# Kernel optimization log

Measured on AMD Instinct MI355X. Metric: run time of the kernel, lower is better.

The kernel has to match this reference:

```python
import jax, jax.numpy as jnp
import numpy as np

K = 20
EPS = 1e-5
SLOPE = 0.2


def setup_inputs() -> dict:
    key = jax.random.key(0)
    k1, k2 = jax.random.split(key, 2)
    B, C, N, O = 2, 64, 8192, 64
    x = jax.random.normal(k1, (B, C, N), dtype=jnp.float32)
    W = jax.random.normal(k2, (O, 2 * C), dtype=jnp.float32) * 0.05  # Conv2d 1x1, bias=False
    gamma = jnp.ones((O,), dtype=jnp.float32)
    beta = jnp.zeros((O,), dtype=jnp.float32)
    return {"x": x, "W": W, "gamma": gamma, "beta": beta}


def reference(x, W, gamma, beta):
    # x: (B, C, N)
    B, C, N = x.shape
    xt = jnp.swapaxes(x, 1, 2)  # (B, N, C)

    # --- get_GraphFeatures: KNN by negative squared euclidean distance ---
    inner = jnp.einsum('bnc,bmc->bnm', xt, xt)          # (B, N, N)
    sq = jnp.sum(xt * xt, axis=-1)                      # (B, N)
    neg_dist = 2.0 * inner - sq[:, :, None] - sq[:, None, :]
    _, idx = jax.lax.top_k(neg_dist, K)                 # (B, N, K) int32

    # gather neighbor features: (B, N, K, C)
    nbr = jax.vmap(lambda pts, i: pts[i])(xt, idx)
    center = xt[:, :, None, :]                          # (B, N, 1, C)
    # edge feature: concat(x_j - x_i, x_i) -> (B, N, K, 2C)
    edge = jnp.concatenate([nbr - center, jnp.broadcast_to(center, nbr.shape)], axis=-1)

    # --- 1x1 conv (pointwise GEMM) -> (B, O, N, K) ---
    h = jnp.einsum('bnkf,of->bonk', edge, W)

    # --- BatchNorm2d (training-mode batch stats over B, N, K per channel) ---
    mean = jnp.mean(h, axis=(0, 2, 3), keepdims=True)
    var = jnp.var(h, axis=(0, 2, 3), keepdims=True)
    h = (h - mean) * jax.lax.rsqrt(var + EPS)
    h = h * gamma[None, :, None, None] + beta[None, :, None, None]

    # --- LeakyReLU(0.2) + max over neighbors ---
    h = jnp.where(h >= 0, h, SLOPE * h)
    return jnp.max(h, axis=-1)                          # (B, O, N)
```

## Files before the change

### kernel.cpp

```cpp
#include <hip/hip_runtime.h>
#include <cfloat>

#define BB 2
#define NN 8192
#define OO 64
#define KK 20
#define QB 128
#define MS 16
#define CHUNK 512
#define CAPQ 192
#define RB 8
#define RBS 9

using f16x8  = __attribute__((ext_vector_type(8))) _Float16;
using f32x16 = __attribute__((ext_vector_type(16))) float;
typedef unsigned long long u64;

#define XH_OFF ((size_t)0)
#define XL_OFF (XH_OFF + (size_t)BB*NN*32)
#define SQ_OFF (XL_OFF + (size_t)BB*NN*32)
#define Y1_OFF (SQ_OFF + (size_t)BB*NN)
#define Y2_OFF (Y1_OFF + (size_t)BB*NN*64)
#define TH_OFF (Y2_OFF + (size_t)BB*NN*64)
#define CN_OFF (TH_OFF + (size_t)BB*NN)
#define TL_OFF (CN_OFF + (size_t)BB*NN)
#define CA_OFF (TL_OFF + (size_t)2*BB*NN*KK)
#define IX_OFF (CA_OFF + (size_t)BB*NN*CAPQ*2)
#define HX_OFF (IX_OFF + (size_t)BB*NN*KK)
#define HN_OFF (HX_OFF + (size_t)BB*NN*64)
#define ST_OFF (HN_OFF + (size_t)BB*NN*64)

__device__ __forceinline__ size_t frag_off(int b, int tile, int t, int lane) {
    return ((((size_t)b * (NN / 32) + tile) * 4 + t) * 64 + lane) * 8;
}

__device__ __forceinline__ unsigned fmap(float f) {
    unsigned u = __float_as_uint(f);
    return (u & 0x80000000u) ? ~u : (u | 0x80000000u);
}

__device__ __forceinline__ void sort16(float* v) {
#pragma unroll
    for (int k = 2; k <= 16; k <<= 1) {
#pragma unroll
        for (int j = k >> 1; j > 0; j >>= 1) {
#pragma unroll
            for (int i = 0; i < 16; ++i) {
                int l = i ^ j;
                if (l > i) {
                    bool up = ((i & k) == 0);
                    float mn = fminf(v[i], v[l]);
                    float mx = fmaxf(v[i], v[l]);
                    v[i] = up ? mn : mx;
                    v[l] = up ? mx : mn;
                }
            }
        }
    }
}
__device__ __forceinline__ void bmerge32(float* A) {
#pragma unroll
    for (int j = 16; j > 0; j >>= 1) {
#pragma unroll
        for (int i = 0; i < 32; ++i) {
            if ((i & j) == 0) {
                float mn = fminf(A[i], A[i | j]);
                float mx = fmaxf(A[i], A[i | j]);
                A[i] = mn;
                A[i | j] = mx;
            }
        }
    }
}
__device__ __forceinline__ void merge32_16(float* A, const float* B) {
#pragma unroll
    for (int i = 16; i < 32; ++i) A[i] = fminf(A[i], B[31 - i]);
    bmerge32(A);
}
__device__ __forceinline__ void merge32_32(float* A, const float* B) {
    float t[32];
#pragma unroll
    for (int i = 0; i < 32; ++i) t[i] = fminf(A[i], B[31 - i]);
    bmerge32(t);
#pragma unroll
    for (int i = 0; i < 32; ++i) A[i] = t[i];
}

__device__ __forceinline__ void load_atile(const _Float16* __restrict__ xh,
                                           const _Float16* __restrict__ xl,
                                           int b, int ptile, int lane,
                                           f16x8* Ah, f16x8* Al) {
#pragma unroll
    for (int t = 0; t < 4; ++t) {
        size_t o = frag_off(b, ptile, t, lane);
        Ah[t] = *(const f16x8*)&xh[o];
        Al[t] = *(const f16x8*)&xl[o];
    }
}

__device__ __forceinline__ void dist_from_frags(const f16x8* Ah, const f16x8* Al,
                                                const float* sqs, int sbase, int kh,
                                                const f16x8* Qh, const f16x8* Ql,
                                                float* dv) {
    f32x16 c0, c1;
#pragma unroll
    for (int r2 = 0; r2 < 4; ++r2) {
        float4 sv = *(const float4*)&sqs[sbase + 8 * r2 + 4 * kh];
        c0[4 * r2 + 0] = sv.x;
        c0[4 * r2 + 1] = sv.y;
        c0[4 * r2 + 2] = sv.z;
        c0[4 * r2 + 3] = sv.w;
    }
#pragma unroll
    for (int i = 0; i < 16; ++i) c1[i] = 0.f;
#pragma unroll
    for (int t = 0; t < 4; ++t) {
        c0 = __builtin_amdgcn_mfma_f32_32x32x16_f16(Ah[t], Qh[t], c0, 0, 0, 0);
        c1 = __builtin_amdgcn_mfma_f32_32x32x16_f16(Ah[t], Ql[t], c1, 0, 0, 0);
        c1 = __builtin_amdgcn_mfma_f32_32x32x16_f16(Al[t], Qh[t], c1, 0, 0, 0);
    }
#pragma unroll
    for (int i = 0; i < 16; ++i)
        dv[i] = fmaf(-2.f, c0[i], -9.765625e-4f * c1[i]);
}

__device__ __forceinline__ void load_qfrag(const _Float16* __restrict__ xh,
                                           const _Float16* __restrict__ xl,
                                           int b, int qbase, int lane,
                                           f16x8* Qh, f16x8* Ql) {
    const int qtile = qbase >> 5;
#pragma unroll
    for (int t = 0; t < 4; ++t) {
        size_t o = frag_off(b, qtile, t, lane);
        Qh[t] = *(const f16x8*)&xh[o];
        Ql[t] = *(const f16x8*)&xl[o];
    }
}

__global__ void __launch_bounds__(256, 2)
kA(const float* __restrict__ x, const float* __restrict__ W,
   float* __restrict__ ws) {
    __shared__ __align__(16) float w1s[32 * 64];
    __shared__ __align__(16) float w2s[32 * 64];
    __shared__ float xs[64 * 65];
    __shared__ float tb[64 * 33];
    const int bb = blockIdx.z;
    const int og = blockIdx.y;
    const int obase = og * 32;
    const int nbase = blockIdx.x * 64;
    const int tn = threadIdx.x & 63, tq = threadIdx.x >> 6;

    for (int i = threadIdx.x; i < 2048; i += 256) {
        int ol = i >> 6, c = i & 63;
        float a = W[(obase + ol) * 128 + c];
        float d = W[(obase + ol) * 128 + 64 + c];
        w1s[i] = a;
        w2s[i] = d - a;
    }
    for (int i = threadIdx.x; i < 4096; i += 256) {
        int c = i >> 6, nl = i & 63;
        xs[c * 65 + nl] = x[((size_t)bb * 64 + c) * NN + nbase + nl];
    }
    if (og == 0) {
        if (blockIdx.x == 0 && bb == 0 && threadIdx.x < 128)
            ws[ST_OFF + threadIdx.x] = 0.f;
        int gid = (bb * 128 + blockIdx.x) * 256 + threadIdx.x;
        if (gid < BB * NN) ((int*)(ws + CN_OFF))[gid] = 0;
    }
    __syncthreads();

    float xc[64];
#pragma unroll
    for (int c = 0; c < 64; ++c) xc[c] = xs[c * 65 + tn];

    if (og == 0 && tq == 0) {
        float sqv = 0.f;
#pragma unroll
        for (int c = 0; c < 64; ++c) sqv = fmaf(xc[c], xc[c], sqv);
        int n = nbase + tn;
        ws[SQ_OFF + (size_t)bb * NN + n] = sqv;
        _Float16* xh = (_Float16*)(ws + XH_OFF);
        _Float16* xl = (_Float16*)(ws + XL_OFF);
        int tile = n >> 5, r = n & 31;
#pragma unroll
        for (int t = 0; t < 4; ++t) {
#pragma unroll
            for (int kh = 0; kh < 2; ++kh) {
                f16x8 vh, vl;
#pragma unroll
                for (int j = 0; j < 8; ++j) {
                    float v = xc[t * 16 + kh * 8 + j];
                    _Float16 h = (_Float16)v;
                    vh[j] = h;
                    vl[j] = (_Float16)((v - (float)h) * 2048.f);
                }
                size_t o = frag_off(bb, tile, t, kh * 32 + r);
                *(f16x8*)&xh[o] = vh;
                *(f16x8*)&xl[o] = vl;
            }
        }
    }

    float a1v[8], a2v[8];
#pragma unroll
    for (int o2 = 0; o2 < 8; ++o2) {
        int ol = tq * 8 + o2;
        const float4* w1v = (const float4*)&w1s[ol * 64];
        const float4* w2v = (const float4*)&w2s[ol * 64];
        float a1 = 0.f, a2 = 0.f;
#pragma unroll
        for (int c4 = 0; c4 < 16; ++c4) {
            float4 v1 = w1v[c4];
            float4 v2 = w2v[c4];
            a1 = fmaf(v1.x, xc[4*c4],   a1);
            a1 = fmaf(v1.y, xc[4*c4+1], a1);
            a1 = fmaf(v1.z, xc[4*c4+2], a1);
            a1 = fmaf(v1.w, xc[4*c4+3], a1);
            a2 = fmaf(v2.x, xc[4*c4],   a2);
            a2 = fmaf(v2.y, xc[4*c4+1], a2);
            a2 = fmaf(v2.z, xc[4*c4+2], a2);
            a2 = fmaf(v2.w, xc[4*c4+3], a2);
        }
        a1v[o2] = a1;
        a2v[o2] = a2;
    }

    const int lo = threadIdx.x & 31;
    const int lp = (threadIdx.x >> 5) & 1;
#pragma unroll
    for (int o2 = 0; o2 < 8; ++o2)
        tb[tn * 33 + tq * 8 + o2] = a1v[o2];
    __syncthreads();
#pragma unroll
    for (int j = 0; j < 8; ++j) {
        int r = tq * 16 + 2 * j + lp;
        ws[Y1_OFF + ((size_t)bb * NN + nbase + r) * 64 + obase + lo] = tb[r * 33 + lo];
    }
    __syncthreads();
#pragma unroll
    for (int o2 = 0; o2 < 8; ++o2)
        tb[tn * 33 + tq * 8 + o2] = a2v[o2];
    __syncthreads();
#pragma unroll
    for (int j = 0; j < 8; ++j) {
        int r = tq * 16 + 2 * j + lp;
        ws[Y2_OFF + ((size_t)bb * NN + nbase + r) * 64 + obase + lo] = tb[r * 33 + lo];
    }
}

__global__ void __launch_bounds__(256, 3)
kT(const _Float16* __restrict__ xh, const _Float16* __restrict__ xl,
   const float* __restrict__ sq, float* __restrict__ thrL) {
    __shared__ float mrg[32 * 128];
    __shared__ __align__(16) float sqs[1024];
    const int tid  = threadIdx.x;
    const int lane = tid & 63;
    const int wv   = tid >> 6;
    const int qcol = lane & 31;
    const int kh   = lane >> 5;
    const int b     = blockIdx.y >> 1;
    const int s     = blockIdx.y & 1;
    const int qbase = blockIdx.x * 32;

    for (int i = tid; i < 1024; i += 256)
        sqs[i] = -0.5f * sq[(size_t)b * NN + s * 1024 + i];

    f16x8 Qh[4], Ql[4];
    load_qfrag(xh, xl, b, qbase, lane, Qh, Ql);
    __syncthreads();

    float dk[32];
#pragma unroll
    for (int i = 0; i < 32; ++i) dk[i] = FLT_MAX;

    const int p0 = s * 1024 + wv * 256;
    for (int pt = p0; pt < p0 + 256; pt += 32) {
        f16x8 Ah[4], Al[4];
        load_atile(xh, xl, b, pt >> 5, lane, Ah, Al);
        float dv[16];
        dist_from_frags(Ah, Al, sqs, pt - s * 1024, kh, Qh, Ql, dv);
        float m16 = dv[0];
#pragma unroll
        for (int i = 1; i < 16; ++i) m16 = fminf(m16, dv[i]);
        if (__any(m16 < dk[KK - 1])) {
            sort16(dv);
            merge32_16(dk, dv);
        }
    }

    {
        float B[32];
#pragma unroll
        for (int j = 0; j < 32; ++j) B[j] = __shfl(dk[j], lane | 32);
        merge32_32(dk, B);
    }
    if (kh == 0) {
#pragma unroll
        for (int j = 0; j < 32; ++j) mrg[j * 128 + wv * 32 + qcol] = dk[j];
    }
    __syncthreads();

    if (tid < 32) {
        float B[32];
#pragma unroll 1
        for (int w = 1; w < 4; ++w) {
#pragma unroll
            for (int j = 0; j < 32; ++j) B[j] = mrg[j * 128 + w * 32 + tid];
            merge32_32(dk, B);
        }
        size_t base = (((size_t)b * 2 + s) * NN + qbase + tid) * KK;
#pragma unroll
        for (int j = 0; j < KK; ++j) thrL[base + j] = dk[j];
    }
}

__global__ void kM2(const float* __restrict__ thrL, float* __restrict__ thr) {
    int gid = blockIdx.x * 256 + threadIdx.x;
    int b = gid >> 13, q = gid & (NN - 1);
    float A[KK], Bv[KK];
    const float4* pa = (const float4*)&thrL[(((size_t)b * 2 + 0) * NN + q) * KK];
    const float4* pb = (const float4*)&thrL[(((size_t)b * 2 + 1) * NN + q) * KK];
#pragma unroll
    for (int i = 0; i < 5; ++i) {
        float4 va = pa[i];
        float4 vb = pb[i];
        A[4*i] = va.x;  A[4*i+1] = va.y;  A[4*i+2] = va.z;  A[4*i+3] = va.w;
        Bv[4*i] = vb.x; Bv[4*i+1] = vb.y; Bv[4*i+2] = vb.z; Bv[4*i+3] = vb.w;
    }
    float v = fminf(Bv[KK - 1], A[KK - 1]);
#pragma unroll
    for (int i = 1; i < KK; ++i)
        v = fminf(v, fmaxf(A[i - 1], Bv[KK - 1 - i]));
    thr[gid] = v + fabsf(v) * 1e-6f + 1e-6f;
}

__global__ void __launch_bounds__(256, 4)
kS(const _Float16* __restrict__ xh, const _Float16* __restrict__ xl,
   const float* __restrict__ sq, const float* __restrict__ thr,
   int* __restrict__ cnt, u64* __restrict__ cand, int tt0) {
    __shared__ u64 lbuf[256 * RBS];
    __shared__ __align__(16) float sqs[CHUNK];
    const int tid  = threadIdx.x;
    const int lane = tid & 63;
    const int wv   = tid >> 6;
    const int qcol = lane & 31;
    const int kh   = lane >> 5;
    const int id     = blockIdx.x;
    const int ychunk = id & 15;
    const int qt     = (id >> 4) & 63;
    const int b      = (id >> 10) & 1;
    const int qbase  = qt * QB + wv * 32;
    const int pbase0 = ychunk * CHUNK;
    const int ptile0 = pbase0 >> 5;

    for (int i = tid; i < CHUNK; i += 256)
        sqs[i] = -0.5f * sq[(size_t)b * NN + pbase0 + i];

    f16x8 Qh[4], Ql[4];
    load_qfrag(xh, xl, b, qbase, lane, Qh, Ql);

    const size_t qidx = (size_t)b * NN + qbase + qcol;
    const float tv = thr[qidx];
    const size_t cb = qidx * CAPQ;
    int c_ = 0;

    __syncthreads();

    auto flushS = [&]() {
        if (c_ > 0) {
            int base = atomicAdd(&cnt[qidx], c_);
#pragma unroll 1
            for (int j = 0; j < c_; ++j) {
                int slot = base + j;
                if (slot < CAPQ) cand[cb + slot] = lbuf[tid * RBS + j];
            }
            c_ = 0;
        }
    };

#pragma unroll 2
    for (int tt = tt0; tt < tt0 + CHUNK / 64; ++tt) {
        f16x8 Ah[4], Al[4];
        load_atile(xh, xl, b, ptile0 + tt, lane, Ah, Al);
        float dv[16];
        dist_from_frags(Ah, Al, sqs, tt * 32, kh, Qh, Ql, dv);

        const int pb4 = pbase0 + tt * 32 + 4 * kh;
#pragma unroll
        for (int i = 0; i < 16; ++i) {
            float d = dv[i];
            if (d <= tv) {
                int id2 = pb4 + ((i & 3) + 8 * (i >> 2));
                lbuf[tid * RBS + c_] = ((u64)fmap(d) << 32) | (unsigned)id2;
                if (++c_ == RB) flushS();
            }
        }
    }
    flushS();
}

__global__ void __launch_bounds__(64)
kP(const int* __restrict__ cnt, const u64* __restrict__ cand,
   int* __restrict__ idxK) {
    const int lane = threadIdx.x;
    const int qloc = lane & 31;
    const int par  = lane >> 5;
    const int q = blockIdx.x * 32 + qloc;
    int m = cnt[q];
    m = m < CAPQ ? m : CAPQ;
    const int nj = (m - par + 1) >> 1;
    u64 kk[KK];
#pragma unroll
    for (int i = 0; i < KK; ++i) kk[i] = ~0ull;

    auto insU = [&](u64 v) {
        kk[KK - 1] = v;
#pragma unroll
        for (int i = KK - 1; i > 0; --i) {
            u64 a = kk[i - 1], c = kk[i];
            bool sw = c < a;
            kk[i - 1] = sw ? c : a;
            kk[i]     = sw ? a : c;
        }
    };

    int jmax = nj;
#pragma unroll
    for (int off = 32; off > 0; off >>= 1) {
        int o = __shfl_xor(jmax, off);
        jmax = o > jmax ? o : jmax;
    }

    const u64* cp = &cand[(size_t)q * CAPQ + par];
#pragma unroll 4
    for (int j = 0; j < jmax; ++j) {
        u64 v = cp[2 * j];
        if ((j < nj) && v < kk[KK - 1]) insU(v);
    }

#pragma unroll
    for (int j = 0; j < KK; ++j) {
        u64 v = __shfl(kk[j], lane | 32);
        bool ins = (par == 0) && v < kk[KK - 1];
        if (!__any(ins)) break;
        if (ins) insU(v);
    }

    if (par == 0) {
        int* op = &idxK[(size_t)q * KK];
#pragma unroll
        for (int i = 0; i < KK; ++i) op[i] = (int)(unsigned)(kk[i] & 0xffffffffu);
    }
}

__global__ void kC1(const float* __restrict__ y1, const float* __restrict__ y2,
                    const int* __restrict__ idxK, float* __restrict__ hmaxT,
                    float* __restrict__ hminT, float* __restrict__ stats) {
    __shared__ int li[32 * KK];
    __shared__ float red[256];
    __shared__ float thm[32 * 65];
    __shared__ float thn[32 * 65];
    int b = blockIdx.y;
    int o = threadIdx.x & 63;
    int nn = threadIdx.x >> 6;
    int nbase = blockIdx.x * 32;

    for (int i = threadIdx.x; i < 32 * KK; i += 256)
        li[i] = idxK[((size_t)b * NN + nbase) * KK + i];
    __syncthreads();

    float s = 0.f, ss = 0.f;
    for (int gidx = 0; gidx < 8; ++gidx) {
        int nl = gidx * 4 + nn;
        int n = nbase + nl;
        float y2v = y2[((size_t)b * NN + n) * 64 + o];
        float hm = -FLT_MAX, hn = FLT_MAX;
        const int* lin = &li[nl * KK];
#pragma unroll 4
        for (int k = 0; k < KK; ++k) {
            int j = lin[k];
            float h = y1[((size_t)b * NN + j) * 64 + o] + y2v;
            s += h;
            ss += h * h;
            hm = fmaxf(hm, h);
            hn = fminf(hn, h);
        }
        thm[nl * 65 + o] = hm;
        thn[nl * 65 + o] = hn;
    }
    __syncthreads();

    int l = threadIdx.x & 31, g = threadIdx.x >> 5;
#pragma unroll
    for (int i = 0; i < 8; ++i) {
        int o2 = g * 8 + i;
        hmaxT[((size_t)b * 64 + o2) * NN + nbase + l] = thm[l * 65 + o2];
        hminT[((size_t)b * 64 + o2) * NN + nbase + l] = thn[l * 65 + o2];
    }

    __syncthreads();
    red[threadIdx.x] = s;
    __syncthreads();
    if (threadIdx.x < 64) {
        float v = red[o] + red[64 + o] + red[128 + o] + red[192 + o];
        atomicAdd(&stats[o], v);
    }
    __syncthreads();
    red[threadIdx.x] = ss;
    __syncthreads();
    if (threadIdx.x < 64) {
        float v = red[o] + red[64 + o] + red[128 + o] + red[192 + o];
        atomicAdd(&stats[64 + o], v);
    }
}

__global__ void kC3(const float* __restrict__ hmaxT, const float* __restrict__ hminT,
                    const float* __restrict__ stats, const float* __restrict__ gamma,
                    const float* __restrict__ beta, float* __restrict__ out) {
    int o = blockIdx.x;
    int half = blockIdx.y;
    int b = blockIdx.z;
    const float c = (float)BB * NN * KK;
    float mean = stats[o] / c;
    float var = stats[64 + o] / c - mean * mean;
    float rs = rsqrtf(var + 1e-5f);
    float a = gamma[o] * rs;
    float b2 = beta[o] - a * mean;
    size_t rowb = ((size_t)b * 64 + o) * NN;
    int n0 = half * (NN / 2), n1 = n0 + NN / 2;
    for (int n = n0 + threadIdx.x; n < n1; n += 256) {
        float hm = hmaxT[rowb + n];
        float hn = hminT[rowb + n];
        float hs = (a >= 0.f) ? hm : hn;
        float v = a * hs + b2;
        v = (v >= 0.f) ? v : 0.2f * v;
        out[rowb + n] = v;
    }
}

extern "C" void kernel_launch(void* const* d_in, const int* in_sizes, int n_in,
                              void* d_out, int out_size, void* d_ws, size_t ws_size,
                              hipStream_t stream) {
    const float* x     = (const float*)d_in[0];
    const float* W     = (const float*)d_in[1];
    const float* gamma = (const float*)d_in[2];
    const float* beta  = (const float*)d_in[3];
    float* out = (float*)d_out;
    float* ws  = (float*)d_ws;

    _Float16* xh = (_Float16*)(ws + XH_OFF);
    _Float16* xl = (_Float16*)(ws + XL_OFF);
    float* sq    = ws + SQ_OFF;
    float* y1    = ws + Y1_OFF;
    float* y2    = ws + Y2_OFF;
    float* thr   = ws + TH_OFF;
    int*   cnt   = (int*)(ws + CN_OFF);
    float* thrL  = ws + TL_OFF;
    u64*   cand  = (u64*)(ws + CA_OFF);
    int*   idxK  = (int*)(ws + IX_OFF);
    float* hmaxT = ws + HX_OFF;
    float* hminT = ws + HN_OFF;
    float* stats = ws + ST_OFF;

    kA<<<dim3(NN / 64, 2, BB), 256, 0, stream>>>(x, W, ws);
    kT<<<dim3(NN / 32, 2 * BB), 256, 0, stream>>>(xh, xl, sq, thrL);
    kM2<<<dim3(BB * NN / 256), 256, 0, stream>>>(thrL, thr);
    kS<<<dim3(MS * (NN / QB) * BB), 256, 0, stream>>>(xh, xl, sq, thr, cnt, cand, 0);
    kS<<<dim3(MS * (NN / QB) * BB), 256, 0, stream>>>(xh, xl, sq, thr, cnt, cand, CHUNK / 64);
    kP<<<dim3(BB * NN / 32), 64, 0, stream>>>(cnt, cand, idxK);
    kC1<<<dim3(NN / 32, BB), 256, 0, stream>>>(y1, y2, idxK, hmaxT, hminT, stats);
    kC3<<<dim3(OO, 2, BB), 256, 0, stream>>>(hmaxT, hminT, stats, gamma, beta, out);
}
```

Baseline: 278.6 us.

## Merge split kS launches and parallelize kP top-K merge across 8 lanes per query

The two kS launches, each covering half of the point chunk, become a single launch that loops over the whole chunk. This removes one launch and reloads of the query fragments and sq staging. kP now uses 8 threads per query instead of 2, each scanning a strided slice of the candidate list, and combines the partial top-K lists with a three-round shuffle tree merge. This shortens the serial insertion-sort chain per thread, at the cost of more merge rounds and heavier register use.

```diff
diff --git a/kernel.cpp b/kernel.cpp
--- a/kernel.cpp
+++ b/kernel.cpp
@@ -337,7 +337,7 @@
 __global__ void __launch_bounds__(256, 4)
 kS(const _Float16* __restrict__ xh, const _Float16* __restrict__ xl,
    const float* __restrict__ sq, const float* __restrict__ thr,
-   int* __restrict__ cnt, u64* __restrict__ cand, int tt0) {
+   int* __restrict__ cnt, u64* __restrict__ cand) {
     __shared__ u64 lbuf[256 * RBS];
     __shared__ __align__(16) float sqs[CHUNK];
     const int tid  = threadIdx.x;
@@ -379,7 +379,7 @@
     };
 
 #pragma unroll 2
-    for (int tt = tt0; tt < tt0 + CHUNK / 64; ++tt) {
+    for (int tt = 0; tt < CHUNK / 32; ++tt) {
         f16x8 Ah[4], Al[4];
         load_atile(xh, xl, b, ptile0 + tt, lane, Ah, Al);
         float dv[16];
@@ -399,16 +399,16 @@
     flushS();
 }
 
-__global__ void __launch_bounds__(64)
+__global__ void __launch_bounds__(256, 2)
 kP(const int* __restrict__ cnt, const u64* __restrict__ cand,
    int* __restrict__ idxK) {
-    const int lane = threadIdx.x;
-    const int qloc = lane & 31;
-    const int par  = lane >> 5;
-    const int q = blockIdx.x * 32 + qloc;
+    const int tid  = threadIdx.x;
+    const int lane = tid & 63;
+    const int s    = tid & 7;
+    const int q    = blockIdx.x * 32 + (tid >> 3);
     int m = cnt[q];
     m = m < CAPQ ? m : CAPQ;
-    const int nj = (m - par + 1) >> 1;
+    const int nj = (m - s + 7) >> 3;
     u64 kk[KK];
 #pragma unroll
     for (int i = 0; i < KK; ++i) kk[i] = ~0ull;
@@ -431,22 +431,27 @@
         jmax = o > jmax ? o : jmax;
     }
 
-    const u64* cp = &cand[(size_t)q * CAPQ + par];
+    const u64* cp = &cand[(size_t)q * CAPQ + s];
 #pragma unroll 4
     for (int j = 0; j < jmax; ++j) {
-        u64 v = cp[2 * j];
+        u64 v = cp[8 * j];
         if ((j < nj) && v < kk[KK - 1]) insU(v);
     }
 
 #pragma unroll
-    for (int j = 0; j < KK; ++j) {
-        u64 v = __shfl(kk[j], lane | 32);
-        bool ins = (par == 0) && v < kk[KK - 1];
-        if (!__any(ins)) break;
-        if (ins) insU(v);
-    }
-
-    if (par == 0) {
+    for (int r = 0; r < 3; ++r) {
+        const int off = 1 << r;
+        const bool act = (s & ((off << 1) - 1)) == 0;
+#pragma unroll
+        for (int j = 0; j < KK; ++j) {
+            u64 v = __shfl(kk[j], lane | off);
+            bool ins = act && v < kk[KK - 1];
+            if (!__any(ins)) break;
+            if (ins) insU(v);
+        }
+    }
+
+    if (s == 0) {
         int* op = &idxK[(size_t)q * KK];
 #pragma unroll
         for (int i = 0; i < KK; ++i) op[i] = (int)(unsigned)(kk[i] & 0xffffffffu);
@@ -565,9 +570,8 @@
     kA<<<dim3(NN / 64, 2, BB), 256, 0, stream>>>(x, W, ws);
     kT<<<dim3(NN / 32, 2 * BB), 256, 0, stream>>>(xh, xl, sq, thrL);
     kM2<<<dim3(BB * NN / 256), 256, 0, stream>>>(thrL, thr);
-    kS<<<dim3(MS * (NN / QB) * BB), 256, 0, stream>>>(xh, xl, sq, thr, cnt, cand, 0);
-    kS<<<dim3(MS * (NN / QB) * BB), 256, 0, stream>>>(xh, xl, sq, thr, cnt, cand, CHUNK / 64);
-    kP<<<dim3(BB * NN / 32), 64, 0, stream>>>(cnt, cand, idxK);
+    kS<<<dim3(MS * (NN / QB) * BB), 256, 0, stream>>>(xh, xl, sq, thr, cnt, cand);
+    kP<<<dim3(BB * NN / 32), 256, 0, stream>>>(cnt, cand, idxK);
     kC1<<<dim3(NN / 32, BB), 256, 0, stream>>>(y1, y2, idxK, hmaxT, hminT, stats);
     kC3<<<dim3(OO, 2, BB), 256, 0, stream>>>(hmaxT, hminT, stats, gamma, beta, out);
 }
```

Measured after the change: 303.3 us. 1.09x slower.
